# Optimization experiments

Measured on AMD Instinct MI355X. Metric: run time of the kernel, lower is better.

The kernel has to match this reference:

```python
import jax, jax.numpy as jnp
import numpy as np

B, N, K = 8, 2048, 16          # clouds, points per cloud, knn k
C_IN, C_OUT, H = 64, 128, 64   # channels; H = hidden of pos_nn/attn_nn MLPs


def _init(key, shape, fan_in):
    return jax.random.normal(key, shape, jnp.float32) / np.sqrt(fan_in)


def setup_inputs() -> dict:
    key = jax.random.key(0)
    ks = jax.random.split(key, 20)
    P = B * N
    inp = {
        "x": jax.random.normal(ks[0], (P, C_IN), jnp.float32),
        "pos": jax.random.uniform(ks[1], (P, 3), jnp.float32),
        "batch": jnp.arange(P, dtype=jnp.int64 if jax.config.jax_enable_x64 else jnp.int32) // N,
        # lin_in: in->in, bias
        "Wi": _init(ks[2], (C_IN, C_IN), C_IN), "bi": jnp.zeros((C_IN,), jnp.float32),
        # PointTransformerConv: lin_src/lin_dst/lin are bias-free Linear(in, out)
        "Wsrc": _init(ks[3], (C_IN, C_OUT), C_IN),
        "Wdst": _init(ks[4], (C_IN, C_OUT), C_IN),
        "Wlin": _init(ks[5], (C_IN, C_OUT), C_IN),
        # pos_nn = MLP([3, 64, out], norm=None, plain_last=False): Lin-ReLU-Lin-ReLU
        "Wp1": _init(ks[6], (3, H), 3), "bp1": jnp.zeros((H,), jnp.float32),
        "Wp2": _init(ks[7], (H, C_OUT), H), "bp2": jnp.zeros((C_OUT,), jnp.float32),
        # attn_nn = MLP([out, 64, out], norm=None, plain_last=False)
        "Wa1": _init(ks[8], (C_OUT, H), C_OUT), "ba1": jnp.zeros((H,), jnp.float32),
        "Wa2": _init(ks[9], (H, C_OUT), H), "ba2": jnp.zeros((C_OUT,), jnp.float32),
        # lin_out: out->out, bias
        "Wo": _init(ks[10], (C_OUT, C_OUT), C_OUT), "bo": jnp.zeros((C_OUT,), jnp.float32),
    }
    return inp


def _knn_with_self(pn):
    # pn: [B,N,3] -> neighbor indices [B,N,K+1] = {self} U kNN (excl self),
    # matching knn_graph(loop=False) followed by conv's add_self_loops.
    sq = jnp.sum(pn * pn, -1)                                   # [B,N]
    d2 = sq[:, :, None] + sq[:, None, :] - 2.0 * jnp.einsum("bnd,bmd->bnm", pn, pn)
    d2 = d2 + jnp.eye(N, dtype=pn.dtype) * 1e10                 # exclude self
    _, idx = jax.lax.top_k(-d2, K)                              # [B,N,K]
    self_idx = jnp.broadcast_to(jnp.arange(N)[None, :, None], (B, N, 1))
    return jnp.concatenate([self_idx, idx], axis=-1)            # [B,N,K+1]


def _forward(x, pos, batch, Wi, bi, Wsrc, Wdst, Wlin, Wp1, bp1, Wp2, bp2,
             Wa1, ba1, Wa2, ba2, Wo, bo):
    # batch is structured as B equal-size clouds of N points (see setup_inputs);
    # knn is computed per-cloud, equivalent to knn_graph(pos, k, batch).
    h = jax.nn.relu(x @ Wi + bi).reshape(B, N, C_IN)            # lin_in + relu
    pn = pos.reshape(B, N, 3)
    nbr = _knn_with_self(pn)                                    # [B,N,K+1]

    gather = jax.vmap(lambda t, i: t[i])                        # [N,C],[N,K+1]->[N,K+1,C]

    a_src = h @ Wsrc                                            # [B,N,C_OUT]
    a_dst = h @ Wdst
    v = h @ Wlin

    rel = pn[:, :, None, :] - gather(pn, nbr)                   # pos_i - pos_j [B,N,K+1,3]
    delta = jax.nn.relu(jax.nn.relu(rel @ Wp1 + bp1) @ Wp2 + bp2)   # pos_nn

    alpha = a_dst[:, :, None, :] - gather(a_src, nbr) + delta   # alpha_i - alpha_j + delta
    attn = jax.nn.relu(jax.nn.relu(alpha @ Wa1 + ba1) @ Wa2 + ba2)  # attn_nn
    w = jax.nn.softmax(attn, axis=2)                            # softmax over neighbors

    msg = w * (gather(v, nbr) + delta)                          # [B,N,K+1,C_OUT]
    out = jnp.mean(msg, axis=2)                                 # aggr='mean' (PyG default here)
    out = out.reshape(B * N, C_OUT)
    return jax.nn.relu(out @ Wo + bo)                           # lin_out + relu


def reference(x, pos, batch, Wi, bi, Wsrc, Wdst, Wlin, Wp1, bp1, Wp2, bp2,
              Wa1, ba1, Wa2, ba2, Wo, bo):
    return _forward(x, pos, batch, Wi, bi, Wsrc, Wdst, Wlin, Wp1, bp1, Wp2, bp2,
                    Wa1, ba1, Wa2, ba2, Wo, bo)
```

## Files before the change

kernel.cpp:

```cpp
#include <hip/hip_runtime.h>
#include <hip/hip_fp16.h>

typedef _Float16 h8 __attribute__((ext_vector_type(8)));
typedef _Float16 h4 __attribute__((ext_vector_type(4)));
typedef float fx4 __attribute__((ext_vector_type(4)));

#define NPTS   2048
#define KP1    17
#define PGPT   4
#define EDGES  68
#define ROWS   80
#define MT     5
#define DELTA_OFF 0
#define PH_OFF    20480
#define ATT_OFF   30720
#define SJ_OFF    30720
#define US_OFF    52224
#define NBR_OFF   53248
#define EDGE_SMEM 53568
#define ATT_RB    168

__device__ __forceinline__ int swzA(int row, int bytecol) {
  return (row << 7) + (bytecol ^ ((row & 7) << 4));
}
__device__ __forceinline__ int swzB(int row, int bytecol) {
  return (row << 8) + (bytecol ^ ((row & 7) << 4));
}

#define KNN_NB   2048
#define GH_NB    256
#define WP_NB    32
#define PK_NB    48
#define P1_GRID  (KNN_NB + GH_NB + WP_NB + PK_NB)

__global__ __launch_bounds__(512) void phase1_kernel(
    const float* __restrict__ pos, int* __restrict__ nbr,
    const float* __restrict__ x, const float* __restrict__ Wi, const float* __restrict__ bi,
    float* __restrict__ h,
    const float* __restrict__ Wdst, const float* __restrict__ Wsrc,
    const float* __restrict__ Wlin, const float* __restrict__ Wa1,
    float* __restrict__ Wall,
    const float* __restrict__ Wp2, const float* __restrict__ Wa2,
    _Float16* __restrict__ p2p, _Float16* __restrict__ a1p, _Float16* __restrict__ a2p)
{
  __shared__ __align__(16) char buf[33792];
  const int bid = blockIdx.x;
  const int tid = threadIdx.x;

  if (bid < KNN_NB) {
    float* px  = (float*)buf;
    float* py  = (float*)(buf + 8192);
    float* pz  = (float*)(buf + 16384);
    float* sqs = (float*)(buf + 24576);
    int p0 = bid * 8;
    int base = (p0 >> 11) << 11;
    for (int i = tid; i < NPTS; i += 512) {
      float xx = pos[(size_t)(base + i) * 3 + 0];
      float yy = pos[(size_t)(base + i) * 3 + 1];
      float zz = pos[(size_t)(base + i) * 3 + 2];
      px[i] = xx; py[i] = yy; pz[i] = zz;
      sqs[i] = xx * xx + yy * yy + zz * zz;
    }
    __syncthreads();
    int wid = tid >> 6, lane = tid & 63;
    int pl = (p0 & 2047) + wid;
    int gp = base + pl;
    float pix = px[pl], piy = py[pl], piz = pz[pl];

    unsigned key[8];
#pragma unroll
    for (int i = 0; i < 8; ++i) key[i] = 0xFFFFFFFFu;
#pragma unroll
    for (int t = 0; t < 32; ++t) {
      int j = t * 64 + lane;
      float dot = pix * px[j] + piy * py[j] + piz * pz[j];
      float dp = __builtin_fmaf(-2.f, dot, sqs[j]) + 4.0f;
      unsigned kb = (__float_as_uint(dp) & 0xFFFFFFE0u) | (unsigned)t;
      kb = (j == pl) ? 0xFFFFFFFFu : kb;
#pragma unroll
      for (int i = 0; i < 8; ++i) {
        unsigned lo = min(key[i], kb), hi = max(key[i], kb);
        key[i] = lo; kb = hi;
      }
    }

    double pxd = (double)pix, pyd = (double)piy, pzd = (double)piz;
    double sqi64 = pxd * pxd + pyd * pyd + pzd * pzd;
    unsigned long long kk[8];
#pragma unroll
    for (int i = 0; i < 8; ++i) {
      if (key[i] == 0xFFFFFFFFu) { kk[i] = 0xFFFFFFFFFFFFFFFFull; continue; }
      int t = key[i] & 31;
      int j = t * 64 + lane;
      double xj = (double)px[j], yj = (double)py[j], zj = (double)pz[j];
      double sqj = xj * xj + yj * yj + zj * zj;
      double dot = pxd * xj + pyd * yj + pzd * zj;
      double d2 = sqi64 + sqj - 2.0 * dot;
      d2 = d2 > 0.0 ? d2 : 0.0;
      unsigned long long bits = (unsigned long long)__double_as_longlong(d2);
      kk[i] = (bits & ~0x7FFull) | (unsigned long long)j;
    }
#define CE(a, b) { unsigned long long lo_ = kk[a] < kk[b] ? kk[a] : kk[b]; \
                   unsigned long long hi_ = kk[a] < kk[b] ? kk[b] : kk[a]; \
                   kk[a] = lo_; kk[b] = hi_; }
    CE(0,1) CE(2,3) CE(4,5) CE(6,7)
    CE(0,2) CE(1,3) CE(4,6) CE(5,7)
    CE(1,2) CE(5,6) CE(0,4) CE(3,7)
    CE(1,5) CE(2,6)
    CE(1,4) CE(3,6)
    CE(2,4) CE(3,5)
    CE(3,4)
#undef CE

    if (lane == 0) nbr[gp * KP1] = gp;
    for (int it = 0; it < 16; ++it) {
      unsigned h32 = (unsigned)(kk[0] >> 32);
      unsigned key2 = (h32 & ~63u) | (unsigned)lane;
      unsigned m2 = key2;
#pragma unroll
      for (int off = 32; off > 0; off >>= 1) {
        unsigned o = __shfl_xor(m2, off);
        m2 = o < m2 ? o : m2;
      }
      bool same = ((key2 ^ m2) >> 6) == 0;
      unsigned long long ball = __ballot(same);
      int wl; unsigned jwin;
      if (__popcll(ball) == 1) {
        wl = (int)(m2 & 63u);
        unsigned lo32 = (unsigned)kk[0];
        unsigned wlo = __shfl(lo32, wl);
        jwin = wlo & 2047u;
      } else {
        unsigned long long mk = same ? kk[0] : 0xFFFFFFFFFFFFFFFFull;
#pragma unroll
        for (int off = 32; off > 0; off >>= 1) {
          unsigned long long o = __shfl_xor(mk, off);
          mk = o < mk ? o : mk;
        }
        jwin = (unsigned)(mk & 2047ull);
        wl = (int)(jwin & 63u);
      }
      if (lane == 0) nbr[gp * KP1 + 1 + it] = base + (int)jwin;
      bool mine = (lane == wl);
#pragma unroll
      for (int i = 0; i < 7; ++i) kk[i] = mine ? kk[i + 1] : kk[i];
      kk[7] = mine ? 0xFFFFFFFFFFFFFFFFull : kk[7];
    }
  } else if (bid < KNN_NB + GH_NB) {
    float* As = (float*)buf;
    float* Ws = (float*)(buf + 64 * 68 * 4);
    int b = bid - KNN_NB;
    long row0 = (long)b * 64;
    {
      int r = tid >> 3, k8 = (tid & 7) * 8;
      float4 a0 = *(const float4*)(x + (row0 + r) * 64 + k8);
      float4 a1 = *(const float4*)(x + (row0 + r) * 64 + k8 + 4);
      *(float4*)&As[r * 68 + k8] = a0;
      *(float4*)&As[r * 68 + k8 + 4] = a1;
      float4 w0 = *(const float4*)(Wi + r * 64 + k8);
      float4 w1 = *(const float4*)(Wi + r * 64 + k8 + 4);
      *(float4*)&Ws[r * 64 + k8] = w0;
      *(float4*)&Ws[r * 64 + k8 + 4] = w1;
    }
    __syncthreads();
    int tx = tid & 15, ty = tid >> 4;
    float acc[2][4] = {};
#pragma unroll 8
    for (int k = 0; k < 64; ++k) {
      float4 w = *(const float4*)&Ws[k * 64 + tx * 4];
      float a0 = As[(ty * 2 + 0) * 68 + k];
      float a1 = As[(ty * 2 + 1) * 68 + k];
      acc[0][0] += a0 * w.x; acc[0][1] += a0 * w.y; acc[0][2] += a0 * w.z; acc[0][3] += a0 * w.w;
      acc[1][0] += a1 * w.x; acc[1][1] += a1 * w.y; acc[1][2] += a1 * w.z; acc[1][3] += a1 * w.w;
    }
    float b0 = bi[tx * 4 + 0], b1 = bi[tx * 4 + 1], b2 = bi[tx * 4 + 2], b3 = bi[tx * 4 + 3];
#pragma unroll
    for (int i = 0; i < 2; ++i) {
      float4 o;
      o.x = fmaxf(acc[i][0] + b0, 0.f); o.y = fmaxf(acc[i][1] + b1, 0.f);
      o.z = fmaxf(acc[i][2] + b2, 0.f); o.w = fmaxf(acc[i][3] + b3, 0.f);
      *(float4*)(h + (row0 + ty * 2 + i) * 64 + tx * 4) = o;
    }
  } else if (bid < KNN_NB + GH_NB + WP_NB) {
    int gid = (bid - KNN_NB - GH_NB) * 512 + tid;
    int q = gid >> 12, r = (gid >> 6) & 63, c = gid & 63;
    float val;
    if (q < 2) {
      const float* W = q ? Wsrc : Wdst;
      float acc = 0.f;
      for (int k = 0; k < 128; ++k) acc += W[r * 128 + k] * Wa1[k * 64 + c];
      val = acc;
    } else {
      val = Wlin[r * 128 + (q - 2) * 64 + c];
    }
    Wall[r * 256 + q * 64 + c] = val;
  } else {
    int gid = (bid - KNN_NB - GH_NB - WP_NB) * 512 + tid;
    int m = gid >> 13;
    int r = gid & 8191;
    int tl = r >> 9;
    int l  = (r >> 3) & 63;
    int j  = r & 7;
    const float* src; _Float16* dst; int N, kt, nt;
    if (m == 0)      { src = Wp2; dst = p2p; N = 128; kt = tl & 1; nt = tl >> 1; }
    else if (m == 1) { src = Wa1; dst = a1p; N = 64;  kt = tl & 3; nt = tl >> 2; }
    else             { src = Wa2; dst = a2p; N = 128; kt = tl & 1; nt = tl >> 1; }
    int k = kt * 32 + (l >> 4) * 8 + j;
    int n = nt * 16 + (l & 15);
    dst[r] = (_Float16)src[k * N + n];
  }
}

template <int KD, bool BIAS, bool RELU>
__global__ __launch_bounds__(256) void gemm_k(
    const float* __restrict__ A, const float* __restrict__ W,
    const float* __restrict__ bias, float* __restrict__ C, int Nfull) {
  __shared__ float As[64][68];
  __shared__ float Ws[64][64];
  int tid = threadIdx.x;
  int tx = tid & 15, ty = tid >> 4;
  long row0 = (long)blockIdx.x * 64;
  int c0 = blockIdx.y * 64;
  float acc[4][4] = {};
  for (int kb = 0; kb < KD; kb += 64) {
    {
      int k4 = (tid & 15) * 4, r = tid >> 4;
#pragma unroll
      for (int rr = 0; rr < 4; ++rr) {
        float4 a = *(const float4*)(A + (row0 + r + rr * 16) * KD + kb + k4);
        As[r + rr * 16][k4 + 0] = a.x; As[r + rr * 16][k4 + 1] = a.y;
        As[r + rr * 16][k4 + 2] = a.z; As[r + rr * 16][k4 + 3] = a.w;
      }
      int c4 = (tid & 15) * 4, kk = tid >> 4;
#pragma unroll
      for (int rr = 0; rr < 4; ++rr) {
        float4 w = *(const float4*)(W + (size_t)(kb + kk + rr * 16) * Nfull + c0 + c4);
        Ws[kk + rr * 16][c4 + 0] = w.x; Ws[kk + rr * 16][c4 + 1] = w.y;
        Ws[kk + rr * 16][c4 + 2] = w.z; Ws[kk + rr * 16][c4 + 3] = w.w;
      }
    }
    __syncthreads();
#pragma unroll 8
    for (int k = 0; k < 64; ++k) {
      float4 w = *(const float4*)&Ws[k][tx * 4];
      float a0 = As[ty * 4 + 0][k], a1 = As[ty * 4 + 1][k];
      float a2 = As[ty * 4 + 2][k], a3 = As[ty * 4 + 3][k];
      acc[0][0] += a0 * w.x; acc[0][1] += a0 * w.y; acc[0][2] += a0 * w.z; acc[0][3] += a0 * w.w;
      acc[1][0] += a1 * w.x; acc[1][1] += a1 * w.y; acc[1][2] += a1 * w.z; acc[1][3] += a1 * w.w;
      acc[2][0] += a2 * w.x; acc[2][1] += a2 * w.y; acc[2][2] += a2 * w.z; acc[2][3] += a2 * w.w;
      acc[3][0] += a3 * w.x; acc[3][1] += a3 * w.y; acc[3][2] += a3 * w.z; acc[3][3] += a3 * w.w;
    }
    __syncthreads();
  }
#pragma unroll
  for (int i = 0; i < 4; ++i) {
    long row = row0 + ty * 4 + i;
    float4 o;
    float b0 = 0, b1 = 0, b2 = 0, b3 = 0;
    if (BIAS) {
      b0 = bias[c0 + tx * 4 + 0]; b1 = bias[c0 + tx * 4 + 1];
      b2 = bias[c0 + tx * 4 + 2]; b3 = bias[c0 + tx * 4 + 3];
    }
    o.x = acc[i][0] + b0; o.y = acc[i][1] + b1; o.z = acc[i][2] + b2; o.w = acc[i][3] + b3;
    if (RELU) { o.x = fmaxf(o.x, 0.f); o.y = fmaxf(o.y, 0.f); o.z = fmaxf(o.z, 0.f); o.w = fmaxf(o.w, 0.f); }
    *(float4*)(C + row * Nfull + c0 + tx * 4) = o;
  }
}

__global__ __launch_bounds__(512, 6) void edge_kernel(
    const float* __restrict__ pos, const int* __restrict__ nbr,
    const float* __restrict__ usv,
    const float* __restrict__ Wp1, const float* __restrict__ bp1,
    const float* __restrict__ bp2, const float* __restrict__ ba1, const float* __restrict__ ba2,
    const _Float16* __restrict__ Wp2p, const _Float16* __restrict__ Wa1p, const _Float16* __restrict__ Wa2p,
    float* __restrict__ out_pre)
{
  __shared__ __align__(16) char smem[EDGE_SMEM];
  int* nbr_s = (int*)(smem + NBR_OFF);
  float* u_s = (float*)(smem + US_OFF);
  const int tid = threadIdx.x;
  const int lane = tid & 63;
  const int wid = tid >> 6;
  const int bid = blockIdx.x;
  const int pb = ((bid & 7) << 9) | (bid >> 3);
  const int p0 = pb * PGPT;

  if (tid < ROWS) nbr_s[tid] = (tid < EDGES) ? nbr[p0 * KP1 + tid] : p0;
  if (tid < PGPT * 64) u_s[tid] = usv[(size_t)(p0 + (tid >> 6)) * 256 + (tid & 63)];
  __syncthreads();

  const int pp5 = tid >> 7;
  const int c5 = tid & 127;
  float vreg[KP1];
#pragma unroll
  for (int k = 0; k < KP1; ++k)
    vreg[k] = usv[(size_t)nbr_s[pp5 * KP1 + k] * 256 + 128 + c5];

  {
    float w1x = Wp1[lane], w1y = Wp1[64 + lane], w1z = Wp1[128 + lane], b1 = bp1[lane];
    for (int e = wid; e < ROWS; e += 8) {
      int ec = min(e, EDGES - 1);
      int j = nbr_s[ec];
      float sv = usv[(size_t)j * 256 + 64 + lane];
      *(_Float16*)(smem + SJ_OFF + swzA(e, lane * 2)) = (_Float16)sv;
      int p = (ec * 241) >> 12;
      int gp = p0 + p;
      float rx = pos[(size_t)gp * 3 + 0] - pos[(size_t)j * 3 + 0];
      float ry = pos[(size_t)gp * 3 + 1] - pos[(size_t)j * 3 + 1];
      float rz = pos[(size_t)gp * 3 + 2] - pos[(size_t)j * 3 + 2];
      float acc = fmaxf(b1 + rx * w1x + ry * w1y + rz * w1z, 0.f);
      *(_Float16*)(smem + PH_OFF + swzA(e, lane * 2)) = (_Float16)acc;
    }
  }
  __syncthreads();

  const int rl = lane & 15;
  const int kl = lane >> 4;

  {
    int nt = wid;
    h8 b0 = *(const h8*)(Wp2p + ((size_t)(nt * 2 + 0) * 64 + lane) * 8);
    h8 b1 = *(const h8*)(Wp2p + ((size_t)(nt * 2 + 1) * 64 + lane) * 8);
    int col = nt * 16 + rl;
    float bias2 = bp2[col];
    for (int mt = 0; mt < MT; ++mt) {
      int arow = mt * 16 + rl;
      h8 a0 = *(const h8*)(smem + PH_OFF + swzA(arow, kl * 16));
      h8 a1 = *(const h8*)(smem + PH_OFF + swzA(arow, 64 + kl * 16));
      fx4 acc = {0.f, 0.f, 0.f, 0.f};
      acc = __builtin_amdgcn_mfma_f32_16x16x32_f16(a0, b0, acc, 0, 0, 0);
      acc = __builtin_amdgcn_mfma_f32_16x16x32_f16(a1, b1, acc, 0, 0, 0);
#pragma unroll
      for (int jj = 0; jj < 4; ++jj) {
        int orow = mt * 16 + kl * 4 + jj;
        float val = fmaxf(acc[jj] + bias2, 0.f);
        *(_Float16*)(smem + DELTA_OFF + swzB(orow, col * 2)) = (_Float16)val;
      }
    }
  }
  __syncthreads();

  {
    int nt = wid & 3;
    h8 b[4];
#pragma unroll
    for (int kt = 0; kt < 4; ++kt)
      b[kt] = *(const h8*)(Wa1p + ((size_t)(nt * 4 + kt) * 64 + lane) * 8);
    int hcol = nt * 16 + rl;
    float b1v = ba1[hcol];
    for (int mt = (wid >> 2); mt < MT; mt += 2) {
      int arow = mt * 16 + rl;
      fx4 acc = {0.f, 0.f, 0.f, 0.f};
#pragma unroll
      for (int kt = 0; kt < 4; ++kt) {
        h8 a = *(const h8*)(smem + DELTA_OFF + swzB(arow, kt * 64 + kl * 16));
        acc = __builtin_amdgcn_mfma_f32_16x16x32_f16(a, b[kt], acc, 0, 0, 0);
      }
#pragma unroll
      for (int jj = 0; jj < 4; ++jj) {
        int orow = mt * 16 + kl * 4 + jj;
        int oc = min(orow, EDGES - 1);
        int p = (oc * 241) >> 12;
        float uu = u_s[p * 64 + hcol];
        float ss = (float)*(const _Float16*)(smem + SJ_OFF + swzA(orow, hcol * 2));
        float val = fmaxf(acc[jj] + uu - ss + b1v, 0.f);
        *(_Float16*)(smem + PH_OFF + swzA(orow, hcol * 2)) = (_Float16)val;
      }
    }
  }
  __syncthreads();

  {
    int nt = wid;
    h8 b0 = *(const h8*)(Wa2p + ((size_t)(nt * 2 + 0) * 64 + lane) * 8);
    h8 b1 = *(const h8*)(Wa2p + ((size_t)(nt * 2 + 1) * 64 + lane) * 8);
    int col = nt * 16 + rl;
    float b2v = ba2[col];
    char* cbase = smem + ATT_OFF + col * ATT_RB;
    for (int mt = 0; mt < MT; ++mt) {
      int arow = mt * 16 + rl;
      h8 a0 = *(const h8*)(smem + PH_OFF + swzA(arow, kl * 16));
      h8 a1 = *(const h8*)(smem + PH_OFF + swzA(arow, 64 + kl * 16));
      fx4 acc = {0.f, 0.f, 0.f, 0.f};
      acc = __builtin_amdgcn_mfma_f32_16x16x32_f16(a0, b0, acc, 0, 0, 0);
      acc = __builtin_amdgcn_mfma_f32_16x16x32_f16(a1, b1, acc, 0, 0, 0);
#pragma unroll
      for (int jj = 0; jj < 4; ++jj) {
        int orow = mt * 16 + kl * 4 + jj;
        if (orow < EDGES) {
          int pp = (orow * 241) >> 12;
          float val = fmaxf(acc[jj] + b2v, 0.f);
          *(_Float16*)(cbase + (orow + 3 * pp) * 2) = (_Float16)val;
        }
      }
    }
  }
  __syncthreads();

  {
    int r0 = pp5 * KP1;
    const char* abase = smem + ATT_OFF + c5 * ATT_RB + pp5 * 40;
    h4 t0 = *(const h4*)(abase + 0);
    h4 t1 = *(const h4*)(abase + 8);
    h4 t2 = *(const h4*)(abase + 16);
    h4 t3 = *(const h4*)(abase + 24);
    float att[KP1];
#pragma unroll
    for (int q = 0; q < 4; ++q) {
      att[0 + q]  = (float)t0[q];
      att[4 + q]  = (float)t1[q];
      att[8 + q]  = (float)t2[q];
      att[12 + q] = (float)t3[q];
    }
    att[16] = (float)*(const _Float16*)(abase + 32);
    float m8[8];
#pragma unroll
    for (int k = 0; k < 8; ++k) m8[k] = fmaxf(att[k], att[k + 8]);
    float m4a = fmaxf(m8[0], m8[1]), m4b = fmaxf(m8[2], m8[3]);
    float m4c = fmaxf(m8[4], m8[5]), m4d = fmaxf(m8[6], m8[7]);
    float m = fmaxf(fmaxf(fmaxf(m4a, m4b), fmaxf(m4c, m4d)), att[16]);
    float den = 0.f;
#pragma unroll
    for (int k = 0; k < KP1; ++k) { att[k] = __expf(att[k] - m); den += att[k]; }
    float inv = 1.f / (den * 17.f);
    float acc = 0.f;
#pragma unroll
    for (int k = 0; k < KP1; ++k) {
      float dd = (float)*(const _Float16*)(smem + DELTA_OFF + swzB(r0 + k, c5 * 2));
      acc += att[k] * (vreg[k] + dd);
    }
    out_pre[(size_t)(p0 + pp5) * 128 + c5] = acc * inv;
  }
}

extern "C" void kernel_launch(void* const* d_in, const int* in_sizes, int n_in,
                              void* d_out, int out_size, void* d_ws, size_t ws_size,
                              hipStream_t stream) {
  const float* x    = (const float*)d_in[0];
  const float* pos  = (const float*)d_in[1];
  const float* Wi   = (const float*)d_in[3];
  const float* bi   = (const float*)d_in[4];
  const float* Wsrc = (const float*)d_in[5];
  const float* Wdst = (const float*)d_in[6];
  const float* Wlin = (const float*)d_in[7];
  const float* Wp1  = (const float*)d_in[8];
  const float* bp1  = (const float*)d_in[9];
  const float* Wp2  = (const float*)d_in[10];
  const float* bp2  = (const float*)d_in[11];
  const float* Wa1  = (const float*)d_in[12];
  const float* ba1  = (const float*)d_in[13];
  const float* Wa2  = (const float*)d_in[14];
  const float* ba2  = (const float*)d_in[15];
  const float* Wo   = (const float*)d_in[16];
  const float* bo   = (const float*)d_in[17];
  float* out = (float*)d_out;

  char* ws = (char*)d_ws;
  float* h    = (float*)(ws + 0);
  float* usv  = (float*)(ws + 4194304);
  float* opre = (float*)(ws + 20971520);
  float* Wall = (float*)(ws + 20971520);
  int*   nbr  = (int*)  (ws + 29360128);
  _Float16* p2p = (_Float16*)(ws + 30474240);
  _Float16* a1p = (_Float16*)(ws + 30490624);
  _Float16* a2p = (_Float16*)(ws + 30507008);

  phase1_kernel<<<P1_GRID, 512, 0, stream>>>(pos, nbr, x, Wi, bi, h,
                                             Wdst, Wsrc, Wlin, Wa1, Wall,
                                             Wp2, Wa2, p2p, a1p, a2p);
  gemm_k<64, false, false><<<dim3(256, 4), 256, 0, stream>>>(h, Wall, nullptr, usv, 256);
  edge_kernel<<<4096, 512, 0, stream>>>(pos, nbr, usv, Wp1, bp1, bp2, ba1, ba2,
                                        p2p, a1p, a2p, opre);
  gemm_k<128, true, true><<<dim3(256, 2), 256, 0, stream>>>(opre, Wo, bo, out, 128);
}
```

Before: 154.0 us.

## Fuse lin_out GEMM into edge kernel and precompute relative positions in kNN

The final lin_out+ReLU GEMM is folded into the edge kernel. The per-point aggregated features are staged in shared memory as fp16 and multiplied by a pre-packed fp16 Wo using MFMA, which removes one kernel launch and the fp32 round trip of the intermediate through global memory. The kNN stage now also writes pos_i - pos_j for each edge, so the edge kernel reads these instead of gathering pos. Neighbor indices are also made wave-uniform with readfirstlane. The trade-offs are fp16 precision in the output projection and extra global writes for the rel buffer.

```diff
diff --git a/kernel.cpp b/kernel.cpp
--- a/kernel.cpp
+++ b/kernel.cpp
@@ -30,7 +30,7 @@
 #define KNN_NB   2048
 #define GH_NB    256
 #define WP_NB    32
-#define PK_NB    48
+#define PK_NB    80
 #define P1_GRID  (KNN_NB + GH_NB + WP_NB + PK_NB)
 
 __global__ __launch_bounds__(512) void phase1_kernel(
@@ -41,7 +41,9 @@
     const float* __restrict__ Wlin, const float* __restrict__ Wa1,
     float* __restrict__ Wall,
     const float* __restrict__ Wp2, const float* __restrict__ Wa2,
-    _Float16* __restrict__ p2p, _Float16* __restrict__ a1p, _Float16* __restrict__ a2p)
+    const float* __restrict__ Wo,
+    _Float16* __restrict__ p2p, _Float16* __restrict__ a1p, _Float16* __restrict__ a2p,
+    _Float16* __restrict__ wop, float* __restrict__ rel)
 {
   __shared__ __align__(16) char buf[33792];
   const int bid = blockIdx.x;
@@ -113,6 +115,7 @@
 #undef CE
 
     if (lane == 0) nbr[gp * KP1] = gp;
+    if (lane < 3)  rel[(size_t)gp * KP1 * 3 + lane] = 0.f;
     for (int it = 0; it < 16; ++it) {
       unsigned h32 = (unsigned)(kk[0] >> 32);
       unsigned key2 = (h32 & ~63u) | (unsigned)lane;
@@ -141,6 +144,11 @@
         wl = (int)(jwin & 63u);
       }
       if (lane == 0) nbr[gp * KP1 + 1 + it] = base + (int)jwin;
+      if (lane < 3) {
+        const float* ps = lane == 0 ? px : (lane == 1 ? py : pz);
+        float pi = lane == 0 ? pix : (lane == 1 ? piy : piz);
+        rel[((size_t)gp * KP1 + 1 + it) * 3 + lane] = pi - ps[(int)jwin];
+      }
       bool mine = (lane == wl);
 #pragma unroll
       for (int i = 0; i < 7; ++i) kk[i] = mine ? kk[i + 1] : kk[i];
@@ -196,18 +204,29 @@
     Wall[r * 256 + q * 64 + c] = val;
   } else {
     int gid = (bid - KNN_NB - GH_NB - WP_NB) * 512 + tid;
-    int m = gid >> 13;
-    int r = gid & 8191;
-    int tl = r >> 9;
-    int l  = (r >> 3) & 63;
-    int j  = r & 7;
-    const float* src; _Float16* dst; int N, kt, nt;
-    if (m == 0)      { src = Wp2; dst = p2p; N = 128; kt = tl & 1; nt = tl >> 1; }
-    else if (m == 1) { src = Wa1; dst = a1p; N = 64;  kt = tl & 3; nt = tl >> 2; }
-    else             { src = Wa2; dst = a2p; N = 128; kt = tl & 1; nt = tl >> 1; }
-    int k = kt * 32 + (l >> 4) * 8 + j;
-    int n = nt * 16 + (l & 15);
-    dst[r] = (_Float16)src[k * N + n];
+    if (gid < 24576) {
+      int m = gid >> 13;
+      int r = gid & 8191;
+      int tl = r >> 9;
+      int l  = (r >> 3) & 63;
+      int j  = r & 7;
+      const float* src; _Float16* dst; int N, kt, nt;
+      if (m == 0)      { src = Wp2; dst = p2p; N = 128; kt = tl & 1; nt = tl >> 1; }
+      else if (m == 1) { src = Wa1; dst = a1p; N = 64;  kt = tl & 3; nt = tl >> 2; }
+      else             { src = Wa2; dst = a2p; N = 128; kt = tl & 1; nt = tl >> 1; }
+      int k = kt * 32 + (l >> 4) * 8 + j;
+      int n = nt * 16 + (l & 15);
+      dst[r] = (_Float16)src[k * N + n];
+    } else {
+      int r = gid - 24576;
+      int tl = r >> 9;
+      int l  = (r >> 3) & 63;
+      int j  = r & 7;
+      int kt = tl & 3, nt = tl >> 2;
+      int k = kt * 32 + (l >> 4) * 8 + j;
+      int n = nt * 16 + (l & 15);
+      wop[r] = (_Float16)Wo[k * 128 + n];
+    }
   }
 }
 
@@ -268,12 +287,14 @@
 }
 
 __global__ __launch_bounds__(512, 6) void edge_kernel(
-    const float* __restrict__ pos, const int* __restrict__ nbr,
+    const int* __restrict__ nbr,
     const float* __restrict__ usv,
+    const float* __restrict__ rel,
     const float* __restrict__ Wp1, const float* __restrict__ bp1,
     const float* __restrict__ bp2, const float* __restrict__ ba1, const float* __restrict__ ba2,
     const _Float16* __restrict__ Wp2p, const _Float16* __restrict__ Wa1p, const _Float16* __restrict__ Wa2p,
-    float* __restrict__ out_pre)
+    const _Float16* __restrict__ Wop, const float* __restrict__ bo,
+    float* __restrict__ out)
 {
   __shared__ __align__(16) char smem[EDGE_SMEM];
   int* nbr_s = (int*)(smem + NBR_OFF);
@@ -293,21 +314,23 @@
   const int c5 = tid & 127;
   float vreg[KP1];
 #pragma unroll
-  for (int k = 0; k < KP1; ++k)
-    vreg[k] = usv[(size_t)nbr_s[pp5 * KP1 + k] * 256 + 128 + c5];
+  for (int k = 0; k < KP1; ++k) {
+    int jv = __builtin_amdgcn_readfirstlane(nbr_s[pp5 * KP1 + k]);
+    vreg[k] = usv[(size_t)jv * 256 + 128 + c5];
+  }
 
   {
     float w1x = Wp1[lane], w1y = Wp1[64 + lane], w1z = Wp1[128 + lane], b1 = bp1[lane];
+    const float* relb = rel + (size_t)p0 * (KP1 * 3);
     for (int e = wid; e < ROWS; e += 8) {
       int ec = min(e, EDGES - 1);
-      int j = nbr_s[ec];
+      int eb = __builtin_amdgcn_readfirstlane(ec);
+      int j = __builtin_amdgcn_readfirstlane(nbr_s[eb]);
       float sv = usv[(size_t)j * 256 + 64 + lane];
       *(_Float16*)(smem + SJ_OFF + swzA(e, lane * 2)) = (_Float16)sv;
-      int p = (ec * 241) >> 12;
-      int gp = p0 + p;
-      float rx = pos[(size_t)gp * 3 + 0] - pos[(size_t)j * 3 + 0];
-      float ry = pos[(size_t)gp * 3 + 1] - pos[(size_t)j * 3 + 1];
-      float rz = pos[(size_t)gp * 3 + 2] - pos[(size_t)j * 3 + 2];
+      float rx = relb[eb * 3 + 0];
+      float ry = relb[eb * 3 + 1];
+      float rz = relb[eb * 3 + 2];
       float acc = fmaxf(b1 + rx * w1x + ry * w1y + rz * w1z, 0.f);
       *(_Float16*)(smem + PH_OFF + swzA(e, lane * 2)) = (_Float16)acc;
     }
@@ -397,6 +420,11 @@
   }
   __syncthreads();
 
+  h8 bw[4];
+#pragma unroll
+  for (int kt = 0; kt < 4; ++kt)
+    bw[kt] = *(const h8*)(Wop + ((size_t)(wid * 4 + kt) * 64 + lane) * 8);
+
   {
     int r0 = pp5 * KP1;
     const char* abase = smem + ATT_OFF + c5 * ATT_RB + pp5 * 40;
@@ -429,7 +457,24 @@
       float dd = (float)*(const _Float16*)(smem + DELTA_OFF + swzB(r0 + k, c5 * 2));
       acc += att[k] * (vreg[k] + dd);
     }
-    out_pre[(size_t)(p0 + pp5) * 128 + c5] = acc * inv;
+    *(_Float16*)(smem + PH_OFF + swzB(pp5, c5 * 2)) = (_Float16)(acc * inv);
+  }
+  __syncthreads();
+
+  {
+    fx4 acc = {0.f, 0.f, 0.f, 0.f};
+#pragma unroll
+    for (int kt = 0; kt < 4; ++kt) {
+      h8 a = *(const h8*)(smem + PH_OFF + swzB(rl, kt * 64 + kl * 16));
+      acc = __builtin_amdgcn_mfma_f32_16x16x32_f16(a, bw[kt], acc, 0, 0, 0);
+    }
+    if (kl == 0) {
+      int col = wid * 16 + rl;
+      float bov = bo[col];
+#pragma unroll
+      for (int jj = 0; jj < 4; ++jj)
+        out[(size_t)(p0 + jj) * 128 + col] = fmaxf(acc[jj] + bov, 0.f);
+    }
   }
 }
 
@@ -458,18 +503,18 @@
   char* ws = (char*)d_ws;
   float* h    = (float*)(ws + 0);
   float* usv  = (float*)(ws + 4194304);
-  float* opre = (float*)(ws + 20971520);
   float* Wall = (float*)(ws + 20971520);
+  float* rel  = (float*)(ws + 21037056);
   int*   nbr  = (int*)  (ws + 29360128);
   _Float16* p2p = (_Float16*)(ws + 30474240);
   _Float16* a1p = (_Float16*)(ws + 30490624);
   _Float16* a2p = (_Float16*)(ws + 30507008);
+  _Float16* wop = (_Float16*)(ws + 30523392);
 
   phase1_kernel<<<P1_GRID, 512, 0, stream>>>(pos, nbr, x, Wi, bi, h,
                                              Wdst, Wsrc, Wlin, Wa1, Wall,
-                                             Wp2, Wa2, p2p, a1p, a2p);
+                                             Wp2, Wa2, Wo, p2p, a1p, a2p, wop, rel);
   gemm_k<64, false, false><<<dim3(256, 4), 256, 0, stream>>>(h, Wall, nullptr, usv, 256);
-  edge_kernel<<<4096, 512, 0, stream>>>(pos, nbr, usv, Wp1, bp1, bp2, ba1, ba2,
-                                        p2p, a1p, a2p, opre);
-  gemm_k<128, true, true><<<dim3(256, 2), 256, 0, stream>>>(opre, Wo, bo, out, 128);
+  edge_kernel<<<4096, 512, 0, stream>>>(nbr, usv, rel, Wp1, bp1, bp2, ba1, ba2,
+                                        p2p, a1p, a2p, wop, bo, out);
 }
```

Result: faster. 143.2 us (-7.0%).
